# Kernel optimization log

Measured on AMD Instinct MI355X. Metric: run time of the kernel, lower is better.

## Reference

```python
import jax, jax.numpy as jnp
import numpy as np

RADIUS = 2          # DKD soft-detection radius -> 5x5 patch
KSIZE = 2 * RADIUS + 1
TEMP = 0.1          # softmax temperature
TOP_K = 2048        # top_k>0 branch: static keypoint count
NMS_R = 3           # simple_nms radius hardcoded in detect_keypoints


def _maxpool(x, r):
    k = 2 * r + 1
    return jax.lax.reduce_window(
        x, -jnp.inf, jax.lax.max,
        (1, 1, k, k), (1, 1, 1, 1),
        ((0, 0), (0, 0), (r, r), (r, r)))


def _maxpool_split(x, r):
    # faithful to max_pool_parallel: pools top/bottom halves independently
    half = x.shape[2] // 2
    return jnp.concatenate([_maxpool(x[:, :, :half], r),
                            _maxpool(x[:, :, half:], r)], axis=2)


def _simple_nms(s, r):
    mm = s == _maxpool_split(s, r)
    for _ in range(2):
        sm = _maxpool_split(mm.astype(s.dtype), r) > 0
        ss = jnp.where(sm, 0.0, s)
        nm = ss == _maxpool_split(ss, r)
        mm = mm | (nm & ~sm)
    return jnp.where(mm, s, 0.0)


def _bilinear(img, xy):
    # grid_sample, mode='bilinear', align_corners=True
    # img: [B,C,H,W], xy: [B,K,2] in [-1,1] (x,y) -> [B,K,C]
    b, c, h, w = img.shape
    imgt = jnp.transpose(img, (0, 2, 3, 1))  # [B,H,W,C]
    x = (xy[..., 0] + 1.0) * 0.5 * (w - 1)
    y = (xy[..., 1] + 1.0) * 0.5 * (h - 1)
    x0 = jnp.floor(x); y0 = jnp.floor(y)
    wx = (x - x0)[..., None]; wy = (y - y0)[..., None]
    x0i = jnp.clip(x0, 0, w - 1).astype(jnp.int32)
    x1i = jnp.clip(x0 + 1, 0, w - 1).astype(jnp.int32)
    y0i = jnp.clip(y0, 0, h - 1).astype(jnp.int32)
    y1i = jnp.clip(y0 + 1, 0, h - 1).astype(jnp.int32)
    bi = jnp.arange(b)[:, None]
    g = lambda yi, xi: imgt[bi, yi, xi]
    return (g(y0i, x0i) * (1 - wx) * (1 - wy) + g(y0i, x1i) * wx * (1 - wy)
            + g(y1i, x0i) * (1 - wx) * wy + g(y1i, x1i) * wx * wy)


def setup_inputs() -> dict:
    key = jax.random.key(0)
    k1, k2 = jax.random.split(key)
    scores_map = jax.random.uniform(k1, (2, 1, 512, 512), dtype=jnp.float32)
    descriptor_map = jax.random.normal(k2, (2, 128, 512, 512), dtype=jnp.float32)
    return {"scores_map": scores_map, "descriptor_map": descriptor_map}


def reference(scores_map, descriptor_map):
    b, _, h, w = scores_map.shape
    r = RADIUS
    dt = scores_map.dtype
    # --- NMS on detached scores ---
    s_ng = jax.lax.stop_gradient(scores_map)
    nms = _simple_nms(s_ng, NMS_R)
    yi = jnp.arange(h); xi = jnp.arange(w)
    border = (((yi >= r + 1) & (yi < h - r))[:, None]
              & ((xi >= r + 1) & (xi < w - r))[None, :])
    nms = nms * border
    # --- top_k keypoint selection (static shape [B,K]) ---
    _, idx = jax.lax.top_k(nms.reshape(b, -1), TOP_K)
    ky = idx // w; kx = idx % w
    # --- gather 5x5 patches (== unfold + fancy index), zero padded ---
    pad = jnp.pad(scores_map[:, 0], ((0, 0), (r, r), (r, r)))
    offs = jnp.arange(KSIZE)
    dyg, dxg = jnp.meshgrid(offs, offs, indexing='ij')
    dy = dyg.reshape(-1); dx = dxg.reshape(-1)           # [25]
    bi = jnp.arange(b)[:, None, None]
    patch = pad[bi, ky[:, :, None] + dy, kx[:, :, None] + dx]   # [B,K,25]
    # hw_grid: (dx, dy) pairs, row-major over (dy, dx) like unfold
    lin = jnp.linspace(-r, r, KSIZE).astype(dt)
    gy, gx = jnp.meshgrid(lin, lin, indexing='ij')
    hw = jnp.stack([gx.reshape(-1), gy.reshape(-1)], axis=-1)   # [25,2]
    # --- soft-argmax subpixel refinement ---
    maxv = jax.lax.stop_gradient(patch.max(-1, keepdims=True))
    xexp = jnp.exp((patch - maxv) / TEMP)
    ssum = xexp.sum(-1)
    xy_res = jnp.einsum('bkp,pc->bkc', xexp, hw) / ssum[..., None]  # [B,K,2]
    d2 = jnp.sum(((hw[None, None] - xy_res[:, :, None]) / r) ** 2, axis=-1)
    disp = (xexp * d2).sum(-1) / ssum                     # [B,K]
    kxy = jnp.stack([kx, ky], axis=-1).astype(dt) + xy_res
    kxy = kxy / jnp.array([w - 1, h - 1], dt) * 2.0 - 1.0  # [-1,1]
    # --- bilinear sampling of scores + descriptors ---
    kptscores = _bilinear(scores_map, kxy)[..., 0]        # [B,K]
    desc = _bilinear(descriptor_map, kxy)                 # [B,K,C]
    desc = desc / jnp.maximum(jnp.linalg.norm(desc, axis=-1, keepdims=True), 1e-12)
    return (kxy, desc, kptscores, disp)
```

## Files before the change

### kernel.cpp

```cpp
#include <hip/hip_runtime.h>
#include <cstdint>
#include <cstddef>

#define H 512
#define W 512
#define NPIX (H * W)
#define TOPK 2048
#define CAND_CAP 4096
#define NBATCH 2

struct Tap {
    int x0, x1, y0, y1;
    float wx, wy;
    float pad0, pad1;
};

__device__ __forceinline__ float mp7f(const float* m, int y, int x) {
    int ylo = y - 3, yhi = y + 3;
    if (y < 256) { if (ylo < 0) ylo = 0; if (yhi > 255) yhi = 255; }
    else         { if (ylo < 256) ylo = 256; if (yhi > 511) yhi = 511; }
    int xlo = x - 3; if (xlo < 0) xlo = 0;
    int xhi = x + 3; if (xhi > 511) xhi = 511;
    float v = -INFINITY;
    for (int yy = ylo; yy <= yhi; ++yy) {
        const float* row = m + yy * W;
        for (int xx = xlo; xx <= xhi; ++xx) v = fmaxf(v, row[xx]);
    }
    return v;
}

__device__ __forceinline__ int any7(const unsigned char* m, int y, int x) {
    int ylo = y - 3, yhi = y + 3;
    if (y < 256) { if (ylo < 0) ylo = 0; if (yhi > 255) yhi = 255; }
    else         { if (ylo < 256) ylo = 256; if (yhi > 511) yhi = 511; }
    int xlo = x - 3; if (xlo < 0) xlo = 0;
    int xhi = x + 3; if (xhi > 511) xhi = 511;
    int v = 0;
    for (int yy = ylo; yy <= yhi; ++yy) {
        const unsigned char* row = m + yy * W;
        for (int xx = xlo; xx <= xhi; ++xx) v |= row[xx];
    }
    return v ? 1 : 0;
}

__global__ void k_mm0(const float* __restrict__ s, unsigned char* __restrict__ mm0) {
    int t = blockIdx.x * blockDim.x + threadIdx.x;
    if (t >= NBATCH * NPIX) return;
    int b = t >> 18;
    int r = t & (NPIX - 1);
    int y = r >> 9, x = r & 511;
    const float* sb = s + (size_t)b * NPIX;
    mm0[t] = (sb[r] == mp7f(sb, y, x)) ? 1 : 0;
}

__global__ void k_suppress(const float* __restrict__ s, const unsigned char* __restrict__ mm,
                           unsigned char* __restrict__ sm, float* __restrict__ ss) {
    int t = blockIdx.x * blockDim.x + threadIdx.x;
    if (t >= NBATCH * NPIX) return;
    int b = t >> 18;
    int r = t & (NPIX - 1);
    int y = r >> 9, x = r & 511;
    int a = any7(mm + (size_t)b * NPIX, y, x);
    sm[t] = (unsigned char)a;
    ss[t] = a ? 0.0f : s[t];
}

__global__ void k_update(const float* __restrict__ ss, const unsigned char* __restrict__ mmin,
                         const unsigned char* __restrict__ sm, unsigned char* __restrict__ mmout) {
    int t = blockIdx.x * blockDim.x + threadIdx.x;
    if (t >= NBATCH * NPIX) return;
    int b = t >> 18;
    int r = t & (NPIX - 1);
    int y = r >> 9, x = r & 511;
    const float* ssb = ss + (size_t)b * NPIX;
    int nm = (ssb[r] == mp7f(ssb, y, x)) ? 1 : 0;
    mmout[t] = (unsigned char)(mmin[t] | (nm & (1 - (int)sm[t])));
}

__global__ void k_final(const float* __restrict__ s, const float* __restrict__ ss,
                        const unsigned char* __restrict__ mm, const unsigned char* __restrict__ sm,
                        float* __restrict__ nms) {
    int t = blockIdx.x * blockDim.x + threadIdx.x;
    if (t >= NBATCH * NPIX) return;
    int b = t >> 18;
    int r = t & (NPIX - 1);
    int y = r >> 9, x = r & 511;
    const float* ssb = ss + (size_t)b * NPIX;
    int nm2 = (ssb[r] == mp7f(ssb, y, x)) ? 1 : 0;
    int mm2 = mm[t] | (nm2 & (1 - (int)sm[t]));
    bool border = (y >= 3) && (y < 510) && (x >= 3) && (x < 510);
    nms[t] = (mm2 && border) ? s[t] : 0.0f;
}

__global__ void k_hist(const float* __restrict__ nms, unsigned int* __restrict__ hist) {
    int t = blockIdx.x * blockDim.x + threadIdx.x;
    if (t >= NBATCH * NPIX) return;
    float v = nms[t];
    if (v > 0.0f) {
        int b = t >> 18;
        unsigned int key = __float_as_uint(v);
        atomicAdd(&hist[b * 65536 + (key >> 16)], 1u);
    }
}

__global__ void k_thresh(const unsigned int* __restrict__ hist, unsigned int* __restrict__ tb) {
    int b = blockIdx.x;
    const unsigned int* h = hist + b * 65536;
    __shared__ unsigned int part[1024];
    int t = threadIdx.x;
    unsigned int acc = 0;
    for (int i = 0; i < 64; ++i) acc += h[t * 64 + i];
    part[t] = acc;
    __syncthreads();
    if (t == 0) {
        unsigned int cum = 0;
        int chunk = 1023;
        for (; chunk >= 0; --chunk) {
            if (cum + part[chunk] >= TOPK) break;
            cum += part[chunk];
        }
        unsigned int bin = 0;
        if (chunk >= 0) {
            int bb = chunk * 64 + 63;
            for (; bb >= chunk * 64; --bb) {
                cum += h[bb];
                if (cum >= TOPK) break;
            }
            if (bb < chunk * 64) bb = chunk * 64;
            bin = (unsigned int)bb;
        }
        tb[b] = bin;
    }
}

__global__ void k_collect(const float* __restrict__ nms, const unsigned int* __restrict__ tb,
                          unsigned long long* __restrict__ cand, unsigned int* __restrict__ cnt) {
    int t = blockIdx.x * blockDim.x + threadIdx.x;
    if (t >= NBATCH * NPIX) return;
    float v = nms[t];
    if (v > 0.0f) {
        int b = t >> 18;
        unsigned int key = __float_as_uint(v);
        if ((key >> 16) >= tb[b]) {
            unsigned int pos = atomicAdd(&cnt[b], 1u);
            if (pos < CAND_CAP) {
                unsigned int pix = (unsigned int)(t & (NPIX - 1));
                cand[b * CAND_CAP + pos] =
                    ((unsigned long long)key << 32) | (unsigned long long)(~pix);
            }
        }
    }
}

__global__ void k_sort(const unsigned long long* __restrict__ cand, const unsigned int* __restrict__ cnt,
                       int* __restrict__ kpts) {
    int b = blockIdx.x;
    __shared__ unsigned long long sk[CAND_CAP];
    int tid = threadIdx.x;
    unsigned int n = cnt[b];
    if (n > CAND_CAP) n = CAND_CAP;
    for (int i = tid; i < CAND_CAP; i += 1024)
        sk[i] = (i < (int)n) ? cand[b * CAND_CAP + i] : 0ULL;
    __syncthreads();
    for (int k = 2; k <= CAND_CAP; k <<= 1) {
        for (int j = k >> 1; j > 0; j >>= 1) {
            for (int i = tid; i < CAND_CAP; i += 1024) {
                int ixj = i ^ j;
                if (ixj > i) {
                    unsigned long long a = sk[i], c = sk[ixj];
                    bool descSeg = ((i & k) == 0);
                    bool doSwap = descSeg ? (a < c) : (a > c);
                    if (doSwap) { sk[i] = c; sk[ixj] = a; }
                }
            }
            __syncthreads();
        }
    }
    for (int r = tid; r < TOPK; r += 1024) {
        unsigned long long c = sk[r];
        unsigned int pix = ~(unsigned int)(c & 0xFFFFFFFFULL);
        kpts[b * TOPK + r] = (int)pix;
    }
}

__global__ void k_soft(const float* __restrict__ s, const int* __restrict__ kpts,
                       float* __restrict__ out_kxy, float* __restrict__ out_sc,
                       float* __restrict__ out_disp, Tap* __restrict__ taps) {
    int t = blockIdx.x * blockDim.x + threadIdx.x;
    if (t >= NBATCH * TOPK) return;
    int b = t >> 11;
    int pix = kpts[t];
    int ky = (pix >> 9) & 511, kx = pix & 511;
    const float* sb = s + (size_t)b * NPIX;

    float p[25];
    float maxv = -INFINITY;
    #pragma unroll
    for (int i = 0; i < 5; ++i)
        #pragma unroll
        for (int j = 0; j < 5; ++j) {
            float v = sb[(ky - 2 + i) * W + (kx - 2 + j)];
            p[i * 5 + j] = v;
            maxv = fmaxf(maxv, v);
        }
    float e[25];
    float ssum = 0.0f, sx = 0.0f, sy = 0.0f;
    #pragma unroll
    for (int i = 0; i < 5; ++i)
        #pragma unroll
        for (int j = 0; j < 5; ++j) {
            float ev = expf((p[i * 5 + j] - maxv) / 0.1f);
            e[i * 5 + j] = ev;
            ssum += ev;
            sx += ev * (float)(j - 2);
            sy += ev * (float)(i - 2);
        }
    float xr = sx / ssum, yr = sy / ssum;
    float acc = 0.0f;
    #pragma unroll
    for (int i = 0; i < 5; ++i)
        #pragma unroll
        for (int j = 0; j < 5; ++j) {
            float dx = ((float)(j - 2) - xr) * 0.5f;
            float dy = ((float)(i - 2) - yr) * 0.5f;
            acc += e[i * 5 + j] * (dx * dx + dy * dy);
        }
    float disp = acc / ssum;

    float nx = ((float)kx + xr) / 511.0f * 2.0f - 1.0f;
    float ny = ((float)ky + yr) / 511.0f * 2.0f - 1.0f;
    out_kxy[t * 2 + 0] = nx;
    out_kxy[t * 2 + 1] = ny;
    out_disp[t] = disp;

    float xp = (nx + 1.0f) * 0.5f * 511.0f;
    float yp = (ny + 1.0f) * 0.5f * 511.0f;
    float x0 = floorf(xp), y0 = floorf(yp);
    float wxf = xp - x0, wyf = yp - y0;
    int x0i = (int)fminf(fmaxf(x0, 0.0f), 511.0f);
    int x1i = (int)fminf(fmaxf(x0 + 1.0f, 0.0f), 511.0f);
    int y0i = (int)fminf(fmaxf(y0, 0.0f), 511.0f);
    int y1i = (int)fminf(fmaxf(y0 + 1.0f, 0.0f), 511.0f);
    float v00 = sb[y0i * W + x0i], v01 = sb[y0i * W + x1i];
    float v10 = sb[y1i * W + x0i], v11 = sb[y1i * W + x1i];
    out_sc[t] = v00 * (1.0f - wxf) * (1.0f - wyf) + v01 * wxf * (1.0f - wyf)
              + v10 * (1.0f - wxf) * wyf + v11 * wxf * wyf;

    Tap tp;
    tp.x0 = x0i; tp.x1 = x1i; tp.y0 = y0i; tp.y1 = y1i;
    tp.wx = wxf; tp.wy = wyf; tp.pad0 = 0.0f; tp.pad1 = 0.0f;
    taps[t] = tp;
}

__global__ void k_desc(const float* __restrict__ dmap, const Tap* __restrict__ taps,
                       float* __restrict__ out_desc) {
    int t = blockIdx.x;
    int b = t >> 11;
    int c = threadIdx.x;
    Tap tp = taps[t];
    const float* db = dmap + ((size_t)(b * 128 + c)) * NPIX;
    float w00 = (1.0f - tp.wx) * (1.0f - tp.wy);
    float w01 = tp.wx * (1.0f - tp.wy);
    float w10 = (1.0f - tp.wx) * tp.wy;
    float w11 = tp.wx * tp.wy;
    float v = db[tp.y0 * W + tp.x0] * w00 + db[tp.y0 * W + tp.x1] * w01
            + db[tp.y1 * W + tp.x0] * w10 + db[tp.y1 * W + tp.x1] * w11;

    float sq = v * v;
    #pragma unroll
    for (int m = 32; m >= 1; m >>= 1) sq += __shfl_xor(sq, m, 64);
    __shared__ float red[2];
    int wave = c >> 6, lane = c & 63;
    if (lane == 0) red[wave] = sq;
    __syncthreads();
    float tot = red[0] + red[1];
    float nrm = sqrtf(tot);
    float sc = 1.0f / fmaxf(nrm, 1e-12f);
    out_desc[(size_t)t * 128 + c] = v * sc;
}

extern "C" void kernel_launch(void* const* d_in, const int* in_sizes, int n_in,
                              void* d_out, int out_size, void* d_ws, size_t ws_size,
                              hipStream_t stream) {
    const float* s    = (const float*)d_in[0];
    const float* dmap = (const float*)d_in[1];
    float* out = (float*)d_out;
    float* out_kxy  = out;
    float* out_desc = out + 8192;
    float* out_sc   = out + 8192 + 524288;
    float* out_disp = out_sc + 4096;

    char* w = (char*)d_ws;
    float* nms           = (float*)w;          w += (size_t)NBATCH * NPIX * 4;
    float* ssb           = (float*)w;          w += (size_t)NBATCH * NPIX * 4;
    unsigned char* mm0   = (unsigned char*)w;  w += (size_t)NBATCH * NPIX;
    unsigned char* mm1   = (unsigned char*)w;  w += (size_t)NBATCH * NPIX;
    unsigned char* smb   = (unsigned char*)w;  w += (size_t)NBATCH * NPIX;
    unsigned int* hist   = (unsigned int*)w;   w += (size_t)NBATCH * 65536 * 4;
    unsigned long long* cand = (unsigned long long*)w; w += (size_t)NBATCH * CAND_CAP * 8;
    unsigned int* cnt    = (unsigned int*)w;   w += 256;
    unsigned int* tb     = (unsigned int*)w;   w += 256;
    int* kpts            = (int*)w;            w += (size_t)NBATCH * TOPK * 4;
    Tap* taps            = (Tap*)w;            w += (size_t)NBATCH * TOPK * sizeof(Tap);

    hipMemsetAsync(hist, 0, (size_t)NBATCH * 65536 * 4, stream);
    hipMemsetAsync(cnt, 0, 256, stream);

    dim3 blk(256);
    dim3 grd((NBATCH * NPIX) / 256);

    k_mm0<<<grd, blk, 0, stream>>>(s, mm0);
    k_suppress<<<grd, blk, 0, stream>>>(s, mm0, smb, ssb);
    k_update<<<grd, blk, 0, stream>>>(ssb, mm0, smb, mm1);
    k_suppress<<<grd, blk, 0, stream>>>(s, mm1, smb, ssb);
    k_final<<<grd, blk, 0, stream>>>(s, ssb, mm1, smb, nms);
    k_hist<<<grd, blk, 0, stream>>>(nms, hist);
    k_thresh<<<dim3(NBATCH), dim3(1024), 0, stream>>>(hist, tb);
    k_collect<<<grd, blk, 0, stream>>>(nms, tb, cand, cnt);
    k_sort<<<dim3(NBATCH), dim3(1024), 0, stream>>>(cand, cnt, kpts);
    k_soft<<<dim3((NBATCH * TOPK) / 256), dim3(256), 0, stream>>>(s, kpts, out_kxy, out_sc, out_disp, taps);
    k_desc<<<dim3(NBATCH * TOPK), dim3(128), 0, stream>>>(dmap, taps, out_desc);
}
```

Measured before the change: 601.4 us.

## Fuse NMS passes into one tiled LDS kernel, parallel threshold scan, rank-based top-k

Replaces the five separate NMS kernels and the histogram kernel with a single tiled kernel. It loads a 62x62 halo tile into shared memory and runs separable 7-wide max/or pools for all suppression iterations, building the histogram inline. The single-thread threshold search becomes a block-wide parallel scan plus a wavefront ballot, and the 4096-element bitonic sort in one block is replaced by a multi-block rank-by-counting selection. This removes several full-image global round trips and serial stages, at the cost of redundant halo compute and O(n^2) comparisons in the rank step.

Result: faster. 509.9 us (-15.2%).

```diff
diff --git a/kernel.cpp b/kernel.cpp
--- a/kernel.cpp
+++ b/kernel.cpp
@@ -9,127 +9,190 @@
 #define CAND_CAP 4096
 #define NBATCH 2
 
+#define RG 62
+#define RS 64
+#define NTOT (RG * RS)
+
 struct Tap {
     int x0, x1, y0, y1;
     float wx, wy;
     float pad0, pad1;
 };
 
-__device__ __forceinline__ float mp7f(const float* m, int y, int x) {
-    int ylo = y - 3, yhi = y + 3;
-    if (y < 256) { if (ylo < 0) ylo = 0; if (yhi > 255) yhi = 255; }
-    else         { if (ylo < 256) ylo = 256; if (yhi > 511) yhi = 511; }
-    int xlo = x - 3; if (xlo < 0) xlo = 0;
-    int xhi = x + 3; if (xhi > 511) xhi = 511;
-    float v = -INFINITY;
-    for (int yy = ylo; yy <= yhi; ++yy) {
-        const float* row = m + yy * W;
-        for (int xx = xlo; xx <= xhi; ++xx) v = fmaxf(v, row[xx]);
-    }
-    return v;
-}
-
-__device__ __forceinline__ int any7(const unsigned char* m, int y, int x) {
-    int ylo = y - 3, yhi = y + 3;
-    if (y < 256) { if (ylo < 0) ylo = 0; if (yhi > 255) yhi = 255; }
-    else         { if (ylo < 256) ylo = 256; if (yhi > 511) yhi = 511; }
-    int xlo = x - 3; if (xlo < 0) xlo = 0;
-    int xhi = x + 3; if (xhi > 511) xhi = 511;
-    int v = 0;
-    for (int yy = ylo; yy <= yhi; ++yy) {
-        const unsigned char* row = m + yy * W;
-        for (int xx = xlo; xx <= xhi; ++xx) v |= row[xx];
-    }
-    return v ? 1 : 0;
-}
-
-__global__ void k_mm0(const float* __restrict__ s, unsigned char* __restrict__ mm0) {
-    int t = blockIdx.x * blockDim.x + threadIdx.x;
-    if (t >= NBATCH * NPIX) return;
-    int b = t >> 18;
-    int r = t & (NPIX - 1);
-    int y = r >> 9, x = r & 511;
+__global__ void k_zero(unsigned int* __restrict__ hist, unsigned int* __restrict__ cnt) {
+    int i = blockIdx.x * 256 + threadIdx.x;
+    if (i < NBATCH * 65536) hist[i] = 0;
+    if (i < 8) cnt[i] = 0;
+}
+
+__global__ __launch_bounds__(256) void k_nms_fused(
+        const float* __restrict__ s, float* __restrict__ nms,
+        unsigned int* __restrict__ hist) {
+    __shared__ float A[NTOT];
+    __shared__ float Bf[NTOT];
+    __shared__ float Cf[NTOT];
+    __shared__ unsigned char Mmm[NTOT];
+    __shared__ unsigned char Msm[NTOT];
+    __shared__ unsigned char Mt[NTOT];
+
+    const int tid = threadIdx.x;
+    const int b = blockIdx.z;
+    const int gx0 = blockIdx.x * 32 - 15;
+    const int gy0 = blockIdx.y * 32 - 15;
+    const int h0 = (blockIdx.y < 8) ? 0 : 256;
+    const int h1 = h0 + 256;
     const float* sb = s + (size_t)b * NPIX;
-    mm0[t] = (sb[r] == mp7f(sb, y, x)) ? 1 : 0;
-}
-
-__global__ void k_suppress(const float* __restrict__ s, const unsigned char* __restrict__ mm,
-                           unsigned char* __restrict__ sm, float* __restrict__ ss) {
-    int t = blockIdx.x * blockDim.x + threadIdx.x;
-    if (t >= NBATCH * NPIX) return;
-    int b = t >> 18;
-    int r = t & (NPIX - 1);
-    int y = r >> 9, x = r & 511;
-    int a = any7(mm + (size_t)b * NPIX, y, x);
-    sm[t] = (unsigned char)a;
-    ss[t] = a ? 0.0f : s[t];
-}
-
-__global__ void k_update(const float* __restrict__ ss, const unsigned char* __restrict__ mmin,
-                         const unsigned char* __restrict__ sm, unsigned char* __restrict__ mmout) {
-    int t = blockIdx.x * blockDim.x + threadIdx.x;
-    if (t >= NBATCH * NPIX) return;
-    int b = t >> 18;
-    int r = t & (NPIX - 1);
-    int y = r >> 9, x = r & 511;
-    const float* ssb = ss + (size_t)b * NPIX;
-    int nm = (ssb[r] == mp7f(ssb, y, x)) ? 1 : 0;
-    mmout[t] = (unsigned char)(mmin[t] | (nm & (1 - (int)sm[t])));
-}
-
-__global__ void k_final(const float* __restrict__ s, const float* __restrict__ ss,
-                        const unsigned char* __restrict__ mm, const unsigned char* __restrict__ sm,
-                        float* __restrict__ nms) {
-    int t = blockIdx.x * blockDim.x + threadIdx.x;
-    if (t >= NBATCH * NPIX) return;
-    int b = t >> 18;
-    int r = t & (NPIX - 1);
-    int y = r >> 9, x = r & 511;
-    const float* ssb = ss + (size_t)b * NPIX;
-    int nm2 = (ssb[r] == mp7f(ssb, y, x)) ? 1 : 0;
-    int mm2 = mm[t] | (nm2 & (1 - (int)sm[t]));
-    bool border = (y >= 3) && (y < 510) && (x >= 3) && (x < 510);
-    nms[t] = (mm2 && border) ? s[t] : 0.0f;
-}
-
-__global__ void k_hist(const float* __restrict__ nms, unsigned int* __restrict__ hist) {
-    int t = blockIdx.x * blockDim.x + threadIdx.x;
-    if (t >= NBATCH * NPIX) return;
-    float v = nms[t];
-    if (v > 0.0f) {
-        int b = t >> 18;
-        unsigned int key = __float_as_uint(v);
-        atomicAdd(&hist[b * 65536 + (key >> 16)], 1u);
-    }
-}
-
-__global__ void k_thresh(const unsigned int* __restrict__ hist, unsigned int* __restrict__ tb) {
+
+    for (int i = tid; i < NTOT; i += 256) {
+        int x = i & 63, y = i >> 6;
+        float v = -INFINITY;
+        int gx = gx0 + x, gy = gy0 + y;
+        if (x < RG && gx >= 0 && gx < W && gy >= h0 && gy < h1)
+            v = sb[gy * W + gx];
+        A[i] = v;
+    }
+    __syncthreads();
+
+    for (int i = tid; i < NTOT; i += 256) {
+        int x = i & 63;
+        if (x >= 3 && x < 59) {
+            float m = A[i - 3];
+            m = fmaxf(m, A[i - 2]); m = fmaxf(m, A[i - 1]); m = fmaxf(m, A[i]);
+            m = fmaxf(m, A[i + 1]); m = fmaxf(m, A[i + 2]); m = fmaxf(m, A[i + 3]);
+            Cf[i] = m;
+        }
+    }
+    __syncthreads();
+
+    for (int i = tid; i < NTOT; i += 256) {
+        int x = i & 63, y = i >> 6;
+        if (x >= 3 && x < 59 && y >= 3 && y < 59) {
+            float m = Cf[i - 3 * RS];
+            m = fmaxf(m, Cf[i - 2 * RS]); m = fmaxf(m, Cf[i - RS]);
+            m = fmaxf(m, Cf[i]);
+            m = fmaxf(m, Cf[i + RS]); m = fmaxf(m, Cf[i + 2 * RS]);
+            m = fmaxf(m, Cf[i + 3 * RS]);
+            Mmm[i] = (A[i] == m) ? 1 : 0;
+        }
+    }
+    __syncthreads();
+
+    for (int it = 0; it < 2; ++it) {
+        const int lo1 = 6 + 6 * it, hi1 = RG - lo1;
+        const int lo0 = lo1 - 3,    hi0 = RG - lo0;
+        const int lo2 = lo1 + 3,    hi2 = RG - lo2;
+
+        for (int i = tid; i < NTOT; i += 256) {
+            int x = i & 63, y = i >> 6;
+            if (x >= lo1 && x < hi1 && y >= lo0 && y < hi0) {
+                Mt[i] = (unsigned char)(Mmm[i - 3] | Mmm[i - 2] | Mmm[i - 1] |
+                                        Mmm[i] | Mmm[i + 1] | Mmm[i + 2] | Mmm[i + 3]);
+            }
+        }
+        __syncthreads();
+
+        for (int i = tid; i < NTOT; i += 256) {
+            int x = i & 63, y = i >> 6;
+            if (x >= lo1 && x < hi1 && y >= lo1 && y < hi1) {
+                unsigned char o = (unsigned char)(Mt[i - 3 * RS] | Mt[i - 2 * RS] |
+                                                  Mt[i - RS] | Mt[i] | Mt[i + RS] |
+                                                  Mt[i + 2 * RS] | Mt[i + 3 * RS]);
+                Msm[i] = o;
+                Bf[i] = o ? 0.0f : A[i];
+            }
+        }
+        __syncthreads();
+
+        for (int i = tid; i < NTOT; i += 256) {
+            int x = i & 63, y = i >> 6;
+            if (x >= lo2 && x < hi2 && y >= lo1 && y < hi1) {
+                float m = Bf[i - 3];
+                m = fmaxf(m, Bf[i - 2]); m = fmaxf(m, Bf[i - 1]); m = fmaxf(m, Bf[i]);
+                m = fmaxf(m, Bf[i + 1]); m = fmaxf(m, Bf[i + 2]); m = fmaxf(m, Bf[i + 3]);
+                Cf[i] = m;
+            }
+        }
+        __syncthreads();
+
+        if (it == 0) {
+            for (int i = tid; i < NTOT; i += 256) {
+                int x = i & 63, y = i >> 6;
+                if (x >= lo2 && x < hi2 && y >= lo2 && y < hi2) {
+                    float m = Cf[i - 3 * RS];
+                    m = fmaxf(m, Cf[i - 2 * RS]); m = fmaxf(m, Cf[i - RS]);
+                    m = fmaxf(m, Cf[i]);
+                    m = fmaxf(m, Cf[i + RS]); m = fmaxf(m, Cf[i + 2 * RS]);
+                    m = fmaxf(m, Cf[i + 3 * RS]);
+                    int nm = (Bf[i] == m) ? 1 : 0;
+                    Mmm[i] = (unsigned char)(Mmm[i] | (nm & (1 - (int)Msm[i])));
+                }
+            }
+            __syncthreads();
+        } else {
+            for (int i = tid; i < NTOT; i += 256) {
+                int x = i & 63, y = i >> 6;
+                if (x >= 15 && x < 47 && y >= 15 && y < 47) {
+                    float m = Cf[i - 3 * RS];
+                    m = fmaxf(m, Cf[i - 2 * RS]); m = fmaxf(m, Cf[i - RS]);
+                    m = fmaxf(m, Cf[i]);
+                    m = fmaxf(m, Cf[i + RS]); m = fmaxf(m, Cf[i + 2 * RS]);
+                    m = fmaxf(m, Cf[i + 3 * RS]);
+                    int nm = (Bf[i] == m) ? 1 : 0;
+                    int mm2 = Mmm[i] | (nm & (1 - (int)Msm[i]));
+                    int gx = gx0 + x, gy = gy0 + y;
+                    bool border = (gx >= 3) && (gx < 510) && (gy >= 3) && (gy < 510);
+                    float v = (mm2 && border) ? A[i] : 0.0f;
+                    nms[(size_t)b * NPIX + gy * W + gx] = v;
+                    if (v > 0.0f) {
+                        unsigned int key = __float_as_uint(v);
+                        atomicAdd(&hist[b * 65536 + (key >> 16)], 1u);
+                    }
+                }
+            }
+        }
+    }
+}
+
+__global__ __launch_bounds__(1024) void k_thresh(const unsigned int* __restrict__ hist,
+                                                 unsigned int* __restrict__ tb) {
     int b = blockIdx.x;
     const unsigned int* h = hist + b * 65536;
-    __shared__ unsigned int part[1024];
+    __shared__ unsigned int scan[1024];
+    __shared__ int cstar;
     int t = threadIdx.x;
+
     unsigned int acc = 0;
-    for (int i = 0; i < 64; ++i) acc += h[t * 64 + i];
-    part[t] = acc;
-    __syncthreads();
-    if (t == 0) {
-        unsigned int cum = 0;
-        int chunk = 1023;
-        for (; chunk >= 0; --chunk) {
-            if (cum + part[chunk] >= TOPK) break;
-            cum += part[chunk];
-        }
-        unsigned int bin = 0;
-        if (chunk >= 0) {
-            int bb = chunk * 64 + 63;
-            for (; bb >= chunk * 64; --bb) {
-                cum += h[bb];
-                if (cum >= TOPK) break;
-            }
-            if (bb < chunk * 64) bb = chunk * 64;
-            bin = (unsigned int)bb;
-        }
-        tb[b] = bin;
+    const uint4* h4 = reinterpret_cast<const uint4*>(h + t * 64);
+    #pragma unroll
+    for (int i = 0; i < 16; ++i) { uint4 v = h4[i]; acc += v.x + v.y + v.z + v.w; }
+    scan[t] = acc;
+    if (t == 0) cstar = -1;
+    __syncthreads();
+    for (int d = 1; d < 1024; d <<= 1) {
+        unsigned int v = (t + d < 1024) ? scan[t + d] : 0;
+        __syncthreads();
+        scan[t] += v;
+        __syncthreads();
+    }
+    unsigned int Snext = (t < 1023) ? scan[t + 1] : 0;
+    if (scan[t] >= TOPK && (t == 1023 || Snext < TOPK)) cstar = t;
+    __syncthreads();
+    int c = cstar;
+    if (c < 0) {
+        if (t == 0) tb[b] = 0;
+        return;
+    }
+    if (t < 64) {
+        unsigned int above = (c < 1023) ? scan[c + 1] : 0;
+        unsigned int suf = h[c * 64 + t];
+        #pragma unroll
+        for (int d = 1; d < 64; d <<= 1) {
+            unsigned int v2 = __shfl_down(suf, d, 64);
+            suf += (t + d < 64) ? v2 : 0;
+        }
+        bool cond = (above + suf) >= (unsigned int)TOPK;
+        unsigned long long msk = __ballot(cond);
+        if (t == 0) tb[b] = (unsigned int)(c * 64 + (63 - __clzll(msk)));
     }
 }
 
@@ -152,34 +215,32 @@
     }
 }
 
-__global__ void k_sort(const unsigned long long* __restrict__ cand, const unsigned int* __restrict__ cnt,
-                       int* __restrict__ kpts) {
-    int b = blockIdx.x;
+__global__ __launch_bounds__(256) void k_rank(const unsigned long long* __restrict__ cand,
+                                              const unsigned int* __restrict__ cnt,
+                                              int* __restrict__ kpts) {
     __shared__ unsigned long long sk[CAND_CAP];
+    int b = blockIdx.y;
     int tid = threadIdx.x;
     unsigned int n = cnt[b];
     if (n > CAND_CAP) n = CAND_CAP;
-    for (int i = tid; i < CAND_CAP; i += 1024)
-        sk[i] = (i < (int)n) ? cand[b * CAND_CAP + i] : 0ULL;
-    __syncthreads();
-    for (int k = 2; k <= CAND_CAP; k <<= 1) {
-        for (int j = k >> 1; j > 0; j >>= 1) {
-            for (int i = tid; i < CAND_CAP; i += 1024) {
-                int ixj = i ^ j;
-                if (ixj > i) {
-                    unsigned long long a = sk[i], c = sk[ixj];
-                    bool descSeg = ((i & k) == 0);
-                    bool doSwap = descSeg ? (a < c) : (a > c);
-                    if (doSwap) { sk[i] = c; sk[ixj] = a; }
-                }
-            }
-            __syncthreads();
-        }
-    }
-    for (int r = tid; r < TOPK; r += 1024) {
-        unsigned long long c = sk[r];
-        unsigned int pix = ~(unsigned int)(c & 0xFFFFFFFFULL);
-        kpts[b * TOPK + r] = (int)pix;
+    const unsigned long long* cb = cand + b * CAND_CAP;
+    for (int i = tid; i < CAND_CAP; i += 256)
+        sk[i] = (i < (int)n) ? cb[i] : 0ULL;
+    __syncthreads();
+    int i = blockIdx.x * 256 + tid;
+    if (i < (int)n) {
+        unsigned long long my = sk[i];
+        int rank = 0;
+        int j = 0;
+        int n4 = (int)n & ~3;
+        for (; j < n4; j += 4) {
+            rank += (sk[j] > my) + (sk[j + 1] > my) + (sk[j + 2] > my) + (sk[j + 3] > my);
+        }
+        for (; j < (int)n; ++j) rank += (sk[j] > my);
+        if (rank < TOPK) {
+            unsigned int pix = ~(unsigned int)(my & 0xFFFFFFFFULL);
+            kpts[b * TOPK + rank] = (int)pix;
+        }
     }
 }
 
@@ -292,10 +353,6 @@
 
     char* w = (char*)d_ws;
     float* nms           = (float*)w;          w += (size_t)NBATCH * NPIX * 4;
-    float* ssb           = (float*)w;          w += (size_t)NBATCH * NPIX * 4;
-    unsigned char* mm0   = (unsigned char*)w;  w += (size_t)NBATCH * NPIX;
-    unsigned char* mm1   = (unsigned char*)w;  w += (size_t)NBATCH * NPIX;
-    unsigned char* smb   = (unsigned char*)w;  w += (size_t)NBATCH * NPIX;
     unsigned int* hist   = (unsigned int*)w;   w += (size_t)NBATCH * 65536 * 4;
     unsigned long long* cand = (unsigned long long*)w; w += (size_t)NBATCH * CAND_CAP * 8;
     unsigned int* cnt    = (unsigned int*)w;   w += 256;
@@ -303,21 +360,11 @@
     int* kpts            = (int*)w;            w += (size_t)NBATCH * TOPK * 4;
     Tap* taps            = (Tap*)w;            w += (size_t)NBATCH * TOPK * sizeof(Tap);
 
-    hipMemsetAsync(hist, 0, (size_t)NBATCH * 65536 * 4, stream);
-    hipMemsetAsync(cnt, 0, 256, stream);
-
-    dim3 blk(256);
-    dim3 grd((NBATCH * NPIX) / 256);
-
-    k_mm0<<<grd, blk, 0, stream>>>(s, mm0);
-    k_suppress<<<grd, blk, 0, stream>>>(s, mm0, smb, ssb);
-    k_update<<<grd, blk, 0, stream>>>(ssb, mm0, smb, mm1);
-    k_suppress<<<grd, blk, 0, stream>>>(s, mm1, smb, ssb);
-    k_final<<<grd, blk, 0, stream>>>(s, ssb, mm1, smb, nms);
-    k_hist<<<grd, blk, 0, stream>>>(nms, hist);
+    k_zero<<<dim3(512), dim3(256), 0, stream>>>(hist, cnt);
+    k_nms_fused<<<dim3(16, 16, NBATCH), dim3(256), 0, stream>>>(s, nms, hist);
     k_thresh<<<dim3(NBATCH), dim3(1024), 0, stream>>>(hist, tb);
-    k_collect<<<grd, blk, 0, stream>>>(nms, tb, cand, cnt);
-    k_sort<<<dim3(NBATCH), dim3(1024), 0, stream>>>(cand, cnt, kpts);
+    k_collect<<<dim3((NBATCH * NPIX) / 256), dim3(256), 0, stream>>>(nms, tb, cand, cnt);
+    k_rank<<<dim3(CAND_CAP / 256, NBATCH), dim3(256), 0, stream>>>(cand, cnt, kpts);
     k_soft<<<dim3((NBATCH * TOPK) / 256), dim3(256), 0, stream>>>(s, kpts, out_kxy, out_sc, out_disp, taps);
     k_desc<<<dim3(NBATCH * TOPK), dim3(128), 0, stream>>>(dmap, taps, out_desc);
 }
```
